# Kernel tuning notes

Measured on AMD Instinct MI355X. Metric: run time of the kernel, lower is better.

## Reference

```python
import jax, jax.numpy as jnp
import numpy as np

N_KERNELS = 5
MUL_FACTOR = 2.0


def setup_inputs() -> dict:
    key = jax.random.key(0)
    X = jax.random.normal(key, (4096, 64), dtype=jnp.float32)
    # bandwidth multipliers: mul_factor ** (arange(K) - K//2)
    bandwidth_multipliers = (MUL_FACTOR ** (jnp.arange(N_KERNELS) - N_KERNELS // 2)).astype(jnp.float32)
    return {"X": X, "bandwidth_multipliers": bandwidth_multipliers}


def reference(X, bandwidth_multipliers):
    # squared pairwise euclidean distances: ||x_i||^2 + ||x_j||^2 - 2 x_i . x_j
    sq_norms = jnp.sum(X * X, axis=-1)                      # [N]
    gram = X @ X.T                                          # [N, N]
    L2 = jnp.maximum(sq_norms[:, None] + sq_norms[None, :] - 2.0 * gram, 0.0)  # [N, N]

    # bandwidth estimate uses .data in torch -> stop_gradient
    n = X.shape[0]
    bw = jax.lax.stop_gradient(L2.sum()) / (n * n - n)

    # sum over K bandwidth-scaled RBF kernels
    scales = bw * bandwidth_multipliers                     # [K]
    out = jnp.sum(jnp.exp(-L2[None, :, :] / scales[:, None, None]), axis=0)  # [N, N]
    return out
```

## Files before the change

kernel.cpp:

```cpp
#include <hip/hip_runtime.h>
#include <hip/hip_bf16.h>
#include <math.h>

#define N 4096
#define PB 32

typedef __attribute__((ext_vector_type(8))) short short8;
typedef __attribute__((ext_vector_type(4))) float floatx4;


__device__ inline unsigned bfpk(float a, float b) {
    unsigned ua = __float_as_uint(a), ub = __float_as_uint(b);
    ua = (ua + 0x7fffu + ((ua >> 16) & 1u)) >> 16;
    ub = (ub + 0x7fffu + ((ub >> 16) & 1u)) >> 16;
    return ua | (ub << 16);
}

__device__ inline uint4 pack8(float4 f0, float4 f1) {
    uint4 r;
    r.x = bfpk(f0.x, f0.y);
    r.y = bfpk(f0.z, f0.w);
    r.z = bfpk(f1.x, f1.y);
    r.w = bfpk(f1.z, f1.w);
    return r;
}

__global__ __launch_bounds__(256) void prep_kernel(const float* __restrict__ X,
                                                   float* __restrict__ ws) {
    __shared__ float sm[256];
    __shared__ float ssum[4];
    const int lane = threadIdx.x & 63, w = threadIdx.x >> 6;
    const int b = blockIdx.x;
    const int row0 = b * 128 + w * 32;
    float mloc = 0.f, Sloc = 0.f;
    #pragma unroll
    for (int rr = 0; rr < 32; ++rr) {
        float x = X[(size_t)(row0 + rr) * 64 + lane];
        mloc += x; Sloc += x * x;
    }
    sm[threadIdx.x] = mloc;
    #pragma unroll
    for (int off = 1; off < 64; off <<= 1) Sloc += __shfl_xor(Sloc, off, 64);
    if (lane == 0) ssum[w] = Sloc;
    __syncthreads();
    if (threadIdx.x < 64) {
        ws[b * 66 + threadIdx.x] =
            sm[threadIdx.x] + sm[64 + threadIdx.x] + sm[128 + threadIdx.x] + sm[192 + threadIdx.x];
    } else if (threadIdx.x == 64) {
        ws[b * 66 + 64] = ssum[0] + ssum[1] + ssum[2] + ssum[3];
    }
}

__global__ __launch_bounds__(256) void rbf_kernel(const float* __restrict__ X,
                                                  const float* __restrict__ ws,
                                                  float* __restrict__ out) {
    __shared__ uint4 lA[512];
    __shared__ uint4 lB[1024];
    __shared__ float sR[64];
    __shared__ float sC[128];

    const int t_ = threadIdx.x;
    const int b  = blockIdx.x;

    int I, J, h;
    if (b < 64) {
        I = J = b >> 1; h = b & 1;
    } else {
        int t = (b - 64) >> 1; h = (b - 64) & 1;
        int i = (int)((63.0f - sqrtf((float)(3969 - 8 * t))) * 0.5f);
        while (31 * (i + 1) - ((i + 1) * i) / 2 <= t) ++i;
        while (31 * i - (i * (i - 1)) / 2 > t) --i;
        int oi = 31 * i - (i * (i - 1)) / 2;
        I = i; J = i + 1 + (t - oi);
    }
    const int rowBase = I * 128 + h * 64;
    const int colBase = J * 128;
    const bool offdiag = (I != J);

    #pragma unroll
    for (int i = 0; i < 4; ++i) {
        int slot = i * 256 + t_;
        int r = slot >> 3, g = slot & 7;
        int c = g ^ (r & 7);
        const float4* p = (const float4*)(X + (size_t)(colBase + r) * 64 + c * 8);
        float4 f0 = p[0], f1 = p[1];
        lB[slot] = pack8(f0, f1);
        float nb = f0.x*f0.x + f0.y*f0.y + f0.z*f0.z + f0.w*f0.w
                 + f1.x*f1.x + f1.y*f1.y + f1.z*f1.z + f1.w*f1.w;
        #pragma unroll
        for (int off = 1; off < 8; off <<= 1) nb += __shfl_xor(nb, off, 64);
        if (g == 0) sC[r] = nb;
    }
    #pragma unroll
    for (int i = 0; i < 2; ++i) {
        int slot = i * 256 + t_;
        int r = slot >> 3, g = slot & 7;
        int c = g ^ (r & 7);
        const float4* p = (const float4*)(X + (size_t)(rowBase + r) * 64 + c * 8);
        float4 f0 = p[0], f1 = p[1];
        lA[slot] = pack8(f0, f1);
        float na = f0.x*f0.x + f0.y*f0.y + f0.z*f0.z + f0.w*f0.w
                 + f1.x*f1.x + f1.y*f1.y + f1.z*f1.z + f1.w*f1.w;
        #pragma unroll
        for (int off = 1; off < 8; off <<= 1) na += __shfl_xor(na, off, 64);
        if (g == 0) sR[r] = na;
    }

    const int lane = t_ & 63;
    float mv = 0.f;
    #pragma unroll 8
    for (int pb = 0; pb < PB; ++pb) mv += ws[pb * 66 + lane];
    float Sv = (lane < PB) ? ws[lane * 66 + 64] : 0.f;
    float mm = mv * mv;
    #pragma unroll
    for (int off = 1; off < 64; off <<= 1) {
        mm += __shfl_xor(mm, off, 64);
        Sv += __shfl_xor(Sv, off, 64);
    }
    float sumL2 = 2.0f * (float)N * Sv - 2.0f * mm;
    const float c1q = -1.4426950408889634f * 0.25f * (float)((size_t)N * N - N) / sumL2;

    __syncthreads();

    const int wave = t_ >> 6;
    const int lr = lane & 15, q = lane >> 4;

    int r1 = wave * 16 + lr;
    short8 a0 = *reinterpret_cast<const short8*>(&lA[8 * r1 + ((q    ) ^ (r1 & 7))]);
    short8 a1 = *reinterpret_cast<const short8*>(&lA[8 * r1 + ((q + 4) ^ (r1 & 7))]);

    floatx4 acc[8];
    #pragma unroll
    for (int tj = 0; tj < 8; ++tj) acc[tj] = (floatx4){0.f, 0.f, 0.f, 0.f};

    #pragma unroll
    for (int tj = 0; tj < 8; ++tj) {
        int r2 = tj * 16 + lr;
        short8 b0 = *reinterpret_cast<const short8*>(&lB[8 * r2 + ((q    ) ^ (r2 & 7))]);
        short8 b1 = *reinterpret_cast<const short8*>(&lB[8 * r2 + ((q + 4) ^ (r2 & 7))]);
        acc[tj] = __builtin_amdgcn_mfma_f32_16x16x32_bf16(a0, b0, acc[tj], 0, 0, 0);
        acc[tj] = __builtin_amdgcn_mfma_f32_16x16x32_bf16(a1, b1, acc[tj], 0, 0, 0);
    }

    const int rb = wave * 16 + q * 4;
    float sr0 = sR[rb], sr1 = sR[rb + 1], sr2 = sR[rb + 2], sr3 = sR[rb + 3];
    #pragma unroll
    for (int tj = 0; tj < 8; ++tj) {
        int cl = tj * 16 + lr;
        float scj = sC[cl];
        size_t col = (size_t)(colBase + cl);
        float4 tp;
        #pragma unroll
        for (int p = 0; p < 4; ++p) {
            float srp = (p == 0) ? sr0 : (p == 1) ? sr1 : (p == 2) ? sr2 : sr3;
            float d2 = srp + scj - 2.0f * acc[tj][p];
            d2 = fmaxf(d2, 0.0f);
            float u  = __builtin_amdgcn_exp2f(d2 * c1q);
            float s1 = u * u;
            float e  = s1 * s1;
            float e2 = e * e;
            float e4 = e2 * e2;
            float val = e4 + e2 + e + s1 + u;
            out[(size_t)(rowBase + rb + p) * N + col] = val;
            ((float*)&tp)[p] = val;
        }
        if (offdiag) {
            *reinterpret_cast<float4*>(&out[col * (size_t)N + (rowBase + rb)]) = tp;
        }
    }
}

extern "C" void kernel_launch(void* const* d_in, const int* in_sizes, int n_in,
                              void* d_out, int out_size, void* d_ws, size_t ws_size,
                              hipStream_t stream) {
    const float* X = (const float*)d_in[0];
    float* out = (float*)d_out;
    float* ws  = (float*)d_ws;

    prep_kernel<<<PB, 256, 0, stream>>>(X, ws);
    rbf_kernel<<<1056, 256, 0, stream>>>(X, ws, out);
}
```

Before: 85.57 us.

## Compute transposed MFMA tile so direct output stores are float4-vectorized

The direct (row-major) output tile is now produced by an MFMA with swapped operands, so each lane holds four consecutive columns of one row and writes them as a single float4 instead of four scalar strided stores. For off-diagonal tiles, the mirrored tile is computed by a second MFMA pass in the original orientation and also stored as float4, which doubles the matrix multiply work for those tiles. Diagonal tiles skip loading the A rows and reuse the already staged B tile. The aim is to cut store instruction count and improve write coalescing, since output bandwidth dominates this kernel.

New measurement: 85.66 us. Within noise of the previous version (+0.1%).

```diff
diff --git a/kernel.cpp b/kernel.cpp
--- a/kernel.cpp
+++ b/kernel.cpp
@@ -62,8 +62,9 @@
     const int t_ = threadIdx.x;
     const int b  = blockIdx.x;
 
+    const bool diag = (b < 64);
     int I, J, h;
-    if (b < 64) {
+    if (diag) {
         I = J = b >> 1; h = b & 1;
     } else {
         int t = (b - 64) >> 1; h = (b - 64) & 1;
@@ -75,7 +76,6 @@
     }
     const int rowBase = I * 128 + h * 64;
     const int colBase = J * 128;
-    const bool offdiag = (I != J);
 
     #pragma unroll
     for (int i = 0; i < 4; ++i) {
@@ -91,19 +91,21 @@
         for (int off = 1; off < 8; off <<= 1) nb += __shfl_xor(nb, off, 64);
         if (g == 0) sC[r] = nb;
     }
-    #pragma unroll
-    for (int i = 0; i < 2; ++i) {
-        int slot = i * 256 + t_;
-        int r = slot >> 3, g = slot & 7;
-        int c = g ^ (r & 7);
-        const float4* p = (const float4*)(X + (size_t)(rowBase + r) * 64 + c * 8);
-        float4 f0 = p[0], f1 = p[1];
-        lA[slot] = pack8(f0, f1);
-        float na = f0.x*f0.x + f0.y*f0.y + f0.z*f0.z + f0.w*f0.w
-                 + f1.x*f1.x + f1.y*f1.y + f1.z*f1.z + f1.w*f1.w;
-        #pragma unroll
-        for (int off = 1; off < 8; off <<= 1) na += __shfl_xor(na, off, 64);
-        if (g == 0) sR[r] = na;
+    if (!diag) {
+        #pragma unroll
+        for (int i = 0; i < 2; ++i) {
+            int slot = i * 256 + t_;
+            int r = slot >> 3, g = slot & 7;
+            int c = g ^ (r & 7);
+            const float4* p = (const float4*)(X + (size_t)(rowBase + r) * 64 + c * 8);
+            float4 f0 = p[0], f1 = p[1];
+            lA[slot] = pack8(f0, f1);
+            float na = f0.x*f0.x + f0.y*f0.y + f0.z*f0.z + f0.w*f0.w
+                     + f1.x*f1.x + f1.y*f1.y + f1.z*f1.z + f1.w*f1.w;
+            #pragma unroll
+            for (int off = 1; off < 8; off <<= 1) na += __shfl_xor(na, off, 64);
+            if (g == 0) sR[r] = na;
+        }
     }
 
     const int lane = t_ & 63;
@@ -124,48 +126,83 @@
 
     const int wave = t_ >> 6;
     const int lr = lane & 15, q = lane >> 4;
-
-    int r1 = wave * 16 + lr;
-    short8 a0 = *reinterpret_cast<const short8*>(&lA[8 * r1 + ((q    ) ^ (r1 & 7))]);
-    short8 a1 = *reinterpret_cast<const short8*>(&lA[8 * r1 + ((q + 4) ^ (r1 & 7))]);
-
-    floatx4 acc[8];
-    #pragma unroll
-    for (int tj = 0; tj < 8; ++tj) acc[tj] = (floatx4){0.f, 0.f, 0.f, 0.f};
-
-    #pragma unroll
-    for (int tj = 0; tj < 8; ++tj) {
-        int r2 = tj * 16 + lr;
-        short8 b0 = *reinterpret_cast<const short8*>(&lB[8 * r2 + ((q    ) ^ (r2 & 7))]);
-        short8 b1 = *reinterpret_cast<const short8*>(&lB[8 * r2 + ((q + 4) ^ (r2 & 7))]);
-        acc[tj] = __builtin_amdgcn_mfma_f32_16x16x32_bf16(a0, b0, acc[tj], 0, 0, 0);
-        acc[tj] = __builtin_amdgcn_mfma_f32_16x16x32_bf16(a1, b1, acc[tj], 0, 0, 0);
-    }
-
-    const int rb = wave * 16 + q * 4;
-    float sr0 = sR[rb], sr1 = sR[rb + 1], sr2 = sR[rb + 2], sr3 = sR[rb + 3];
-    #pragma unroll
-    for (int tj = 0; tj < 8; ++tj) {
-        int cl = tj * 16 + lr;
-        float scj = sC[cl];
-        size_t col = (size_t)(colBase + cl);
-        float4 tp;
-        #pragma unroll
-        for (int p = 0; p < 4; ++p) {
-            float srp = (p == 0) ? sr0 : (p == 1) ? sr1 : (p == 2) ? sr2 : sr3;
-            float d2 = srp + scj - 2.0f * acc[tj][p];
-            d2 = fmaxf(d2, 0.0f);
-            float u  = __builtin_amdgcn_exp2f(d2 * c1q);
-            float s1 = u * u;
-            float e  = s1 * s1;
-            float e2 = e * e;
-            float e4 = e2 * e2;
-            float val = e4 + e2 + e + s1 + u;
-            out[(size_t)(rowBase + rb + p) * N + col] = val;
-            ((float*)&tp)[p] = val;
-        }
-        if (offdiag) {
-            *reinterpret_cast<float4*>(&out[col * (size_t)N + (rowBase + rb)]) = tp;
+    const int rl = wave * 16 + lr;
+
+    short8 a0, a1;
+    if (diag) {
+        int rr = h * 64 + rl;
+        a0 = *reinterpret_cast<const short8*>(&lB[8 * rr + ((q    ) ^ (rr & 7))]);
+        a1 = *reinterpret_cast<const short8*>(&lB[8 * rr + ((q + 4) ^ (rr & 7))]);
+    } else {
+        a0 = *reinterpret_cast<const short8*>(&lA[8 * rl + ((q    ) ^ (rl & 7))]);
+        a1 = *reinterpret_cast<const short8*>(&lA[8 * rl + ((q + 4) ^ (rl & 7))]);
+    }
+    const float rnorm = diag ? sC[h * 64 + rl] : sR[rl];
+
+    {
+        floatx4 acc[8];
+        #pragma unroll
+        for (int tj = 0; tj < 8; ++tj) acc[tj] = (floatx4){0.f, 0.f, 0.f, 0.f};
+        #pragma unroll
+        for (int tj = 0; tj < 8; ++tj) {
+            int r2 = tj * 16 + lr;
+            short8 b0 = *reinterpret_cast<const short8*>(&lB[8 * r2 + ((q    ) ^ (r2 & 7))]);
+            short8 b1 = *reinterpret_cast<const short8*>(&lB[8 * r2 + ((q + 4) ^ (r2 & 7))]);
+            acc[tj] = __builtin_amdgcn_mfma_f32_16x16x32_bf16(b0, a0, acc[tj], 0, 0, 0);
+            acc[tj] = __builtin_amdgcn_mfma_f32_16x16x32_bf16(b1, a1, acc[tj], 0, 0, 0);
+        }
+        float* orow = out + (size_t)(rowBase + rl) * N + colBase;
+        #pragma unroll
+        for (int tj = 0; tj < 8; ++tj) {
+            int c0 = tj * 16 + q * 4;
+            float4 v;
+            #pragma unroll
+            for (int p = 0; p < 4; ++p) {
+                float d2 = rnorm + sC[c0 + p] - 2.0f * acc[tj][p];
+                d2 = fmaxf(d2, 0.0f);
+                float u  = __builtin_amdgcn_exp2f(d2 * c1q);
+                float s1 = u * u;
+                float e  = s1 * s1;
+                float e2 = e * e;
+                float e4 = e2 * e2;
+                ((float*)&v)[p] = e4 + e2 + e + s1 + u;
+            }
+            *reinterpret_cast<float4*>(orow + c0) = v;
+        }
+    }
+
+    if (!diag) {
+        floatx4 acc[8];
+        #pragma unroll
+        for (int tj = 0; tj < 8; ++tj) acc[tj] = (floatx4){0.f, 0.f, 0.f, 0.f};
+        #pragma unroll
+        for (int tj = 0; tj < 8; ++tj) {
+            int r2 = tj * 16 + lr;
+            short8 b0 = *reinterpret_cast<const short8*>(&lB[8 * r2 + ((q    ) ^ (r2 & 7))]);
+            short8 b1 = *reinterpret_cast<const short8*>(&lB[8 * r2 + ((q + 4) ^ (r2 & 7))]);
+            acc[tj] = __builtin_amdgcn_mfma_f32_16x16x32_bf16(a0, b0, acc[tj], 0, 0, 0);
+            acc[tj] = __builtin_amdgcn_mfma_f32_16x16x32_bf16(a1, b1, acc[tj], 0, 0, 0);
+        }
+        const int rb = wave * 16 + q * 4;
+        float n0 = sR[rb], n1 = sR[rb + 1], n2 = sR[rb + 2], n3 = sR[rb + 3];
+        #pragma unroll
+        for (int tj = 0; tj < 8; ++tj) {
+            int cl = tj * 16 + lr;
+            float cn = sC[cl];
+            float4 v;
+            #pragma unroll
+            for (int p = 0; p < 4; ++p) {
+                float srp = (p == 0) ? n0 : (p == 1) ? n1 : (p == 2) ? n2 : n3;
+                float d2 = srp + cn - 2.0f * acc[tj][p];
+                d2 = fmaxf(d2, 0.0f);
+                float u  = __builtin_amdgcn_exp2f(d2 * c1q);
+                float s1 = u * u;
+                float e  = s1 * s1;
+                float e2 = e * e;
+                float e4 = e2 * e2;
+                ((float*)&v)[p] = e4 + e2 + e + s1 + u;
+            }
+            *reinterpret_cast<float4*>(out + (size_t)(colBase + cl) * N + rowBase + rb) = v;
         }
     }
 }
```
